# Kernel tuning notes

Measured on AMD Instinct MI355X. Metric: run time of the kernel, lower is better.

The kernel has to match this reference:

```python
import jax, jax.numpy as jnp
import numpy as np
from jax import lax

NPOINT = 1024
NSAMPLES = (16, 32, 64)
BN_EPS = 1e-5


def fps(xyz, npoint):
    """Farthest point sampling. xyz: [B,N,3] -> idx [B,npoint].
    Deterministic start at index 0 (torch version uses a random start)."""
    B, N, _ = xyz.shape

    def step(carry, _):
        dist, far = carry
        centroid = jnp.take_along_axis(xyz, far[:, None, None], axis=1)  # [B,1,3]
        d = jnp.sum((xyz - centroid) ** 2, axis=-1)                      # [B,N]
        dist = jnp.minimum(dist, d)
        nxt = jnp.argmax(dist, axis=1)
        return (dist, nxt), far

    init = (jnp.full((B, N), 1e10, xyz.dtype), jnp.zeros((B,), jnp.int32))
    _, idxs = lax.scan(step, init, None, length=npoint)  # [npoint,B]
    return idxs.T


def gather_points(points, idx):
    # points [B,N,C], idx [B,...] -> [B,...,C]
    return jax.vmap(lambda p, i: p[i])(points, idx)


def sq_cdist(a, b):
    # a [B,S,3], b [B,N,3] -> squared distances [B,S,N] (same ordering as cdist)
    aa = jnp.sum(a * a, -1)[:, :, None]
    bb = jnp.sum(b * b, -1)[:, None, :]
    return aa + bb - 2.0 * jnp.einsum('bsc,bnc->bsn', a, b)


def mlp_scale(g, ws, gs, bs):
    # g: [B,S,k,Cin]; 1x1 conv + BatchNorm (training-mode stats) + ReLU per layer
    for w, gm, bt in zip(ws, gs, bs):
        g = jnp.einsum('bskc,oc->bsko', g, w)
        mu = jnp.mean(g, axis=(0, 1, 2))
        var = jnp.var(g, axis=(0, 1, 2))
        g = jax.nn.relu((g - mu) * lax.rsqrt(var + BN_EPS) * gm + bt)
    return g


def setup_inputs() -> dict:
    key = jax.random.key(0)
    ks = jax.random.split(key, 16)
    B, N, C = 16, 4096, 64
    xyz = jax.random.normal(ks[0], (B, N, 3), jnp.float32)
    features = jax.random.normal(ks[1], (B, N, C), jnp.float32)
    # stacked per-scale MLP params; layer dims: 67 -> 64 -> 64 -> 128
    w0 = jax.random.normal(ks[2], (3, 64, 67), jnp.float32) * 0.1
    w1 = jax.random.normal(ks[3], (3, 64, 64), jnp.float32) * 0.1
    w2 = jax.random.normal(ks[4], (3, 128, 64), jnp.float32) * 0.1
    g0 = jnp.ones((3, 64), jnp.float32); b0 = jnp.zeros((3, 64), jnp.float32)
    g1 = jnp.ones((3, 64), jnp.float32); b1 = jnp.zeros((3, 64), jnp.float32)
    g2 = jnp.ones((3, 128), jnp.float32); b2 = jnp.zeros((3, 128), jnp.float32)
    return {"xyz": xyz, "features": features, "w0": w0, "w1": w1, "w2": w2,
            "g0": g0, "g1": g1, "g2": g2, "b0": b0, "b1": b1, "b2": b2}


def reference(xyz, features, w0, w1, w2, g0, g1, g2, b0, b1, b2):
    fps_idx = fps(xyz, NPOINT)                                   # [B,S]
    new_xyz = jnp.take_along_axis(xyz, fps_idx[..., None], axis=1)  # [B,S,3]
    d2 = sq_cdist(new_xyz, xyz)                                  # [B,S,N]
    outs = []
    for s, nsample in enumerate(NSAMPLES):
        _, idx = lax.top_k(-d2, nsample)                         # k nearest, [B,S,k]
        grouped_xyz = gather_points(xyz, idx) - new_xyz[:, :, None, :]
        grouped_f = gather_points(features, idx)
        g = jnp.concatenate([grouped_xyz, grouped_f], axis=-1)   # [B,S,k,67]
        g = mlp_scale(g, (w0[s], w1[s], w2[s]), (g0[s], g1[s], g2[s]), (b0[s], b1[s], b2[s]))
        outs.append(jnp.max(g, axis=2))                          # max over neighbors -> [B,S,128]
    fused = jnp.concatenate(outs, axis=-1)                       # [B,S,384]
    return new_xyz, fused
```

## Files before the change

kernel.cpp:

```cpp
#include <hip/hip_runtime.h>
#include <stdint.h>

#define BATCH 16
#define NPTS  4096
#define NSAMP 1024

typedef __attribute__((ext_vector_type(8))) short  short8;
typedef __attribute__((ext_vector_type(4))) float  floatx4;

__device__ __forceinline__ unsigned short f2bf(float f) {
    unsigned u = __float_as_uint(f);
    unsigned r = (u + 0x7FFFu + ((u >> 16) & 1u)) >> 16;
    return (unsigned short)r;
}

template<int CTRL>
__device__ __forceinline__ uint64_t dpp_max_u64(uint64_t k) {
    int lo = (int)(unsigned)k;
    int hi = (int)(unsigned)(k >> 32);
    int lo2 = __builtin_amdgcn_update_dpp(0, lo, CTRL, 0xF, 0xF, false);
    int hi2 = __builtin_amdgcn_update_dpp(0, hi, CTRL, 0xF, 0xF, false);
    uint64_t o = ((uint64_t)(unsigned)hi2 << 32) | (unsigned)lo2;
    return o > k ? o : k;
}

__global__ __launch_bounds__(512) void fps_conv_kernel(
    const float* __restrict__ xyz,
    float* __restrict__ out_xyz,
    const float* __restrict__ feat,
    unsigned short* __restrict__ featb,
    int staged)
{
#pragma clang fp contract(off)
    if (blockIdx.x >= 16) {
        if (staged) {
            int t = (blockIdx.x - 16) * 512 + threadIdx.x;
            const float4* fp = (const float4*)feat + (size_t)t*2;
            float4 a = fp[0], c = fp[1];
            uint4 o;
            o.x = (unsigned)f2bf(a.x) | ((unsigned)f2bf(a.y) << 16);
            o.y = (unsigned)f2bf(a.z) | ((unsigned)f2bf(a.w) << 16);
            o.z = (unsigned)f2bf(c.x) | ((unsigned)f2bf(c.y) << 16);
            o.w = (unsigned)f2bf(c.z) | ((unsigned)f2bf(c.w) << 16);
            ((uint4*)featb)[t] = o;
        }
        return;
    }

    const int b    = blockIdx.x;
    const int tid  = threadIdx.x;
    const int lane = tid & 63;
    const int wave = tid >> 6;
    const float* xb = xyz + (size_t)b * NPTS * 3;

    __shared__ float xsh[NPTS], ysh[NPTS], zsh[NPTS];
    __shared__ float cents[NSAMP * 3];
    __shared__ uint64_t keylds[2][8];

    float px[8], py[8], pz[8], dist[8];
    unsigned nidx[8];
#pragma unroll
    for (int i = 0; i < 8; ++i) {
        int p = tid + (i << 9);
        px[i] = xb[p*3+0];
        py[i] = xb[p*3+1];
        pz[i] = xb[p*3+2];
        dist[i] = 1e10f;
        nidx[i] = ~(unsigned)p;
        xsh[p] = px[i]; ysh[p] = py[i]; zsh[p] = pz[i];
    }
    __syncthreads();

    float cx = xb[0], cy = xb[1], cz = xb[2];

    for (int it = 0; it < NSAMP; ++it) {
        if (tid == 0) {
            cents[it*3+0] = cx; cents[it*3+1] = cy; cents[it*3+2] = cz;
        }
        if (it == NSAMP - 1) break;

        uint64_t k[8];
#pragma unroll
        for (int i = 0; i < 8; ++i) {
            float dx = px[i] - cx, dy = py[i] - cy, dz = pz[i] - cz;
            float d = dx*dx; d = d + dy*dy; d = d + dz*dz;
            float nd = fminf(dist[i], d);
            dist[i] = nd;
            k[i] = ((uint64_t)__float_as_uint(nd) << 32) | nidx[i];
        }
        uint64_t m0 = k[0] > k[1] ? k[0] : k[1];
        uint64_t m1 = k[2] > k[3] ? k[2] : k[3];
        uint64_t m2 = k[4] > k[5] ? k[4] : k[5];
        uint64_t m3 = k[6] > k[7] ? k[6] : k[7];
        uint64_t ma = m0 > m1 ? m0 : m1;
        uint64_t mb = m2 > m3 ? m2 : m3;
        uint64_t kk = ma > mb ? ma : mb;

        kk = dpp_max_u64<0x121>(kk);
        kk = dpp_max_u64<0x122>(kk);
        kk = dpp_max_u64<0x124>(kk);
        kk = dpp_max_u64<0x128>(kk);
        kk = dpp_max_u64<0x142>(kk);
        kk = dpp_max_u64<0x143>(kk);

        int pb = it & 1;
        if (lane == 63) keylds[pb][wave] = kk;
        __syncthreads();

        uint64_t f = keylds[pb][lane & 7];
        f = dpp_max_u64<0x121>(f);
        f = dpp_max_u64<0x122>(f);
        f = dpp_max_u64<0x124>(f);
        int cur = (int)~((unsigned)f);

        cx = xsh[cur]; cy = ysh[cur]; cz = zsh[cur];
    }

    __syncthreads();
    for (int i = tid; i < NSAMP*3; i += 512)
        out_xyz[(size_t)b*NSAMP*3 + i] = cents[i];
}

#define WT_S 18432

__global__ __launch_bounds__(256) void conv_w_kernel(
    const float* __restrict__ w0, const float* __restrict__ w1,
    const float* __restrict__ w2, unsigned short* __restrict__ wtab)
{
    int t = blockIdx.x * 256 + threadIdx.x;
    if (t >= 3*WT_S) return;
    int s = t / WT_S, r = t % WT_S;
    unsigned short v = 0;
    if (r < 6144) {
        int n = r / 96, kg = r % 96;
        if (kg < 67) {
            int ci = (kg < 64) ? (kg + 3) : (kg - 64);
            v = f2bf(w0[(size_t)(s*64 + n)*67 + ci]);
        }
    } else if (r < 10240) {
        int idx = r - 6144;
        v = f2bf(w1[(size_t)(s*64 + (idx >> 6))*64 + (idx & 63)]);
    } else {
        int idx = r - 10240;
        v = f2bf(w2[(size_t)(s*128 + (idx >> 6))*64 + (idx & 63)]);
    }
    wtab[t] = v;
}

__global__ __launch_bounds__(256) void knn_kernel(
    const float* __restrict__ xyz,
    const float* __restrict__ new_xyz,
    unsigned short* __restrict__ knn_idx)
{
#pragma clang fp contract(off)
    __shared__ float xs[NPTS], ys[NPTS], zs[NPTS];
    __shared__ uint64_t buf[4][64];
    const int tid  = threadIdx.x;
    const int lane = tid & 63;
    const int wave = tid >> 6;
    const int q = blockIdx.x * 4 + wave;
    const int b = q >> 10;
    const float* xb = xyz + (size_t)b * NPTS * 3;

    for (int i = tid; i < NPTS; i += 256) {
        xs[i] = xb[i*3+0];
        ys[i] = xb[i*3+1];
        zs[i] = xb[i*3+2];
    }
    __syncthreads();

    const float qx = new_xyz[q*3+0], qy = new_xyz[q*3+1], qz = new_xyz[q*3+2];
    float aa = qx*qx; aa = aa + qy*qy; aa = aa + qz*qz;

    auto keyof = [&](int c) -> unsigned {
        float x = xs[c], y = ys[c], z = zs[c];
        float bb = x*x;  bb = bb + y*y;   bb = bb + z*z;
        float dt = qx*x; dt = dt + qy*y;  dt = dt + qz*z;
        float d2 = (aa + bb) - 2.0f*dt;
        unsigned u = __float_as_uint(d2);
        return (u & 0x80000000u) ? ~u : (u | 0x80000000u);
    };
    auto shfl64 = [&](uint64_t v, int src) -> uint64_t {
        int lo = __shfl((int)(unsigned)v, src);
        int hi = __shfl((int)(unsigned)(v >> 32), src);
        return ((uint64_t)(unsigned)hi << 32) | (unsigned)lo;
    };
    auto shflx64 = [&](uint64_t v, int m) -> uint64_t {
        int lo = __shfl_xor((int)(unsigned)v, m);
        int hi = __shfl_xor((int)(unsigned)(v >> 32), m);
        return ((uint64_t)(unsigned)hi << 32) | (unsigned)lo;
    };
    auto sortP = [&](uint64_t &p) {
#pragma unroll
        for (int kk = 2; kk <= 64; kk <<= 1) {
#pragma unroll
            for (int j = kk >> 1; j >= 1; j >>= 1) {
                uint64_t o = shflx64(p, j);
                bool up    = ((lane & kk) == 0);
                bool lower = ((lane & j) == 0);
                bool oless = o < p;
                bool keep  = (up == lower) ? oless : !oless;
                if (keep) p = o;
            }
        }
    };
    auto mergeP = [&](uint64_t &P, uint64_t Bv) {
        uint64_t rev = shfl64(Bv, 63 - lane);
        if (rev < P) P = rev;
#pragma unroll
        for (int j = 32; j >= 1; j >>= 1) {
            uint64_t o = shflx64(P, j);
            bool lower = ((lane & j) == 0);
            bool oless = o < P;
            bool keep  = lower ? oless : !oless;
            if (keep) P = o;
        }
    };

    uint64_t P = ((uint64_t)keyof(lane) << 32) | (unsigned)lane;
    sortP(P);
    uint64_t Pmax = shfl64(P, 63);
    int cnt = 0;

    for (int bt = 1; bt < 64; ++bt) {
        int c = (bt << 6) + lane;
        uint64_t cand = ((uint64_t)keyof(c) << 32) | (unsigned)c;
        bool qual = cand < Pmax;
        unsigned long long mask = __ballot(qual);
        if (mask == 0ull) continue;
        int n = __popcll(mask);
        if (cnt + n > 64) {
            uint64_t Bv = (lane < cnt) ? buf[wave][lane] : ~0ull;
            sortP(Bv);
            mergeP(P, Bv);
            Pmax = shfl64(P, 63);
            cnt = 0;
            qual = qual && (cand < Pmax);
            mask = __ballot(qual);
            n = __popcll(mask);
        }
        if (qual) {
            int pos = cnt + __popcll(mask & ((1ull << lane) - 1ull));
            buf[wave][pos] = cand;
        }
        cnt += n;
    }
    if (cnt > 0) {
        uint64_t Bv = (lane < cnt) ? buf[wave][lane] : ~0ull;
        sortP(Bv);
        mergeP(P, Bv);
    }
    knn_idx[(size_t)q*64 + lane] = (unsigned short)(P & 0xFFFFu);
}

#define GPB 8

template<int PHASE>
__global__ __launch_bounds__(256) void mlp_phase(
    const float* __restrict__ xyz,
    const float* __restrict__ feat,
    const float* __restrict__ new_xyz,
    const unsigned short* __restrict__ knn,
    const unsigned short* __restrict__ featb,
    int staged,
    const unsigned short* __restrict__ wtab,
    const float* __restrict__ bnp,
    float* __restrict__ stats,
    float* __restrict__ out1)
{
    __shared__ __align__(16) unsigned short g_lds[64*104];
    __shared__ __align__(16) unsigned short a_lds[64*72];
    __shared__ float stat_lds[256];
    __shared__ float wavemax[4*128];

    const int tid  = threadIdx.x;
    const int lane = tid & 63;
    const int wave = tid >> 6;
    const int n16  = lane & 15;
    const int quad = lane >> 4;

    int scale, g0;
    {
        int blk = blockIdx.x;
        if (blk < 512)       { scale = 0; g0 = blk * GPB; }
        else if (blk < 1536) { scale = 1; g0 = (blk - 512) * GPB; }
        else                 { scale = 2; g0 = (blk - 1536) * GPB; }
    }
    const int KNB = 16 << scale;
    const int cpg = 4 >> scale;
    const int wpc = 1 << scale;

    const unsigned short* wt  = wtab + scale * WT_S;
    const unsigned short* w2b = wt + 6144;
    const unsigned short* w3b = wt + 10240;

    short8 w1f[4][3];
#pragma unroll
    for (int nt = 0; nt < 4; ++nt)
#pragma unroll
        for (int kb = 0; kb < 3; ++kb)
            w1f[nt][kb] = *(const short8*)&wt[(nt*16 + n16)*96 + kb*32 + quad*8];

    float s1p[4], t1p[4], s2p[4], t2p[4];
    if constexpr (PHASE >= 2) {
#pragma unroll
        for (int nt = 0; nt < 4; ++nt) {
            int o = ((0*3 + scale)*128 + nt*16 + n16)*2;
            s1p[nt] = bnp[o]; t1p[nt] = bnp[o+1];
        }
    }
    if constexpr (PHASE >= 3) {
#pragma unroll
        for (int nt = 0; nt < 4; ++nt) {
            int o = ((1*3 + scale)*128 + nt*16 + n16)*2;
            s2p[nt] = bnp[o]; t2p[nt] = bnp[o+1];
        }
    }

    float sac[8], sqac[8];
#pragma unroll
    for (int i = 0; i < 8; ++i) { sac[i] = 0.f; sqac[i] = 0.f; }
    stat_lds[tid] = 0.f;
    {
        const int r = tid >> 2;
        const int sub = tid & 3;
        if (sub == 0)      *(uint4*)&g_lds[r*104 + 72] = make_uint4(0u,0u,0u,0u);
        else if (sub == 1) *(uint4*)&g_lds[r*104 + 80] = make_uint4(0u,0u,0u,0u);
        else if (sub == 2) *(uint4*)&g_lds[r*104 + 88] = make_uint4(0u,0u,0u,0u);
    }
    __syncthreads();

    for (int g = g0; g < g0 + GPB; ++g) {
        const int cb = g * cpg;
        {
            const int r   = tid >> 2;
            const int sub = tid & 3;
            const int ci  = cb + (r >> (4 + scale));
            const int j   = r & (KNB - 1);
            const int n   = knn[(size_t)ci*64 + j];
            const int b   = ci >> 10;
            if (staged) {
                const unsigned short* frow = featb + ((size_t)(b*NPTS + n))*64 + sub*16;
                uint4 c0 = ((const uint4*)frow)[0];
                uint4 c1 = ((const uint4*)frow)[1];
                *(uint4*)&g_lds[r*104 + sub*16]     = c0;
                *(uint4*)&g_lds[r*104 + sub*16 + 8] = c1;
            } else {
                const float* frow = feat + ((size_t)(b*NPTS + n))*64 + sub*16;
                unsigned short h[16];
#pragma unroll
                for (int u = 0; u < 16; ++u) h[u] = f2bf(frow[u]);
                uint4 p0, p1;
                p0.x = (unsigned)h[0]  | ((unsigned)h[1]  << 16);
                p0.y = (unsigned)h[2]  | ((unsigned)h[3]  << 16);
                p0.z = (unsigned)h[4]  | ((unsigned)h[5]  << 16);
                p0.w = (unsigned)h[6]  | ((unsigned)h[7]  << 16);
                p1.x = (unsigned)h[8]  | ((unsigned)h[9]  << 16);
                p1.y = (unsigned)h[10] | ((unsigned)h[11] << 16);
                p1.z = (unsigned)h[12] | ((unsigned)h[13] << 16);
                p1.w = (unsigned)h[14] | ((unsigned)h[15] << 16);
                *(uint4*)&g_lds[r*104 + sub*16]     = p0;
                *(uint4*)&g_lds[r*104 + sub*16 + 8] = p1;
            }
            if (sub == 0) {
                const float* nx = new_xyz + (size_t)ci*3;
                const float* xp = xyz + ((size_t)(b*NPTS + n))*3;
                unsigned short h0 = f2bf(xp[0] - nx[0]);
                unsigned short h1 = f2bf(xp[1] - nx[1]);
                unsigned short h2 = f2bf(xp[2] - nx[2]);
                uint4 z = make_uint4((unsigned)h0 | ((unsigned)h1 << 16),
                                     (unsigned)h2, 0u, 0u);
                *(uint4*)&g_lds[r*104 + 64] = z;
            }
        }
        __syncthreads();

        const int rb = wave*16 + n16;
        short8 a0 = *(const short8*)&g_lds[rb*104 +      quad*8];
        short8 a1 = *(const short8*)&g_lds[rb*104 + 32 + quad*8];
        short8 a2 = *(const short8*)&g_lds[rb*104 + 64 + quad*8];
        floatx4 acc[4];
#pragma unroll
        for (int nt = 0; nt < 4; ++nt) {
            floatx4 c = {0.f,0.f,0.f,0.f};
            c = __builtin_amdgcn_mfma_f32_16x16x32_bf16(a0, w1f[nt][0], c, 0,0,0);
            c = __builtin_amdgcn_mfma_f32_16x16x32_bf16(a1, w1f[nt][1], c, 0,0,0);
            c = __builtin_amdgcn_mfma_f32_16x16x32_bf16(a2, w1f[nt][2], c, 0,0,0);
            acc[nt] = c;
        }

        if constexpr (PHASE == 1) {
#pragma unroll
            for (int nt = 0; nt < 4; ++nt) {
                floatx4 c = acc[nt];
                sac[nt]  += c[0]+c[1]+c[2]+c[3];
                sqac[nt] += c[0]*c[0]+c[1]*c[1]+c[2]*c[2]+c[3]*c[3];
            }
        }
        if constexpr (PHASE >= 2) {
#pragma unroll
            for (int nt = 0; nt < 4; ++nt) {
                int ch = nt*16 + n16;
#pragma unroll
                for (int r = 0; r < 4; ++r) {
                    float v = acc[nt][r]*s1p[nt] + t1p[nt];
                    v = fmaxf(v, 0.f);
                    a_lds[(wave*16 + quad*4 + r)*72 + ch] = f2bf(v);
                }
            }
            short8 e0 = *(const short8*)&a_lds[rb*72 +      quad*8];
            short8 e1 = *(const short8*)&a_lds[rb*72 + 32 + quad*8];
            floatx4 acc2[4];
#pragma unroll
            for (int nt = 0; nt < 4; ++nt) {
                short8 wa = *(const short8*)&w2b[(nt*16 + n16)*64 +      quad*8];
                short8 wb = *(const short8*)&w2b[(nt*16 + n16)*64 + 32 + quad*8];
                floatx4 c = {0.f,0.f,0.f,0.f};
                c = __builtin_amdgcn_mfma_f32_16x16x32_bf16(e0, wa, c, 0,0,0);
                c = __builtin_amdgcn_mfma_f32_16x16x32_bf16(e1, wb, c, 0,0,0);
                acc2[nt] = c;
            }
            if constexpr (PHASE == 2) {
#pragma unroll
                for (int nt = 0; nt < 4; ++nt) {
                    floatx4 c = acc2[nt];
                    sac[nt]  += c[0]+c[1]+c[2]+c[3];
                    sqac[nt] += c[0]*c[0]+c[1]*c[1]+c[2]*c[2]+c[3]*c[3];
                }
            }
            if constexpr (PHASE == 3) {
#pragma unroll
                for (int nt = 0; nt < 4; ++nt) {
                    int ch = nt*16 + n16;
#pragma unroll
                    for (int r = 0; r < 4; ++r) {
                        float v = acc2[nt][r]*s2p[nt] + t2p[nt];
                        v = fmaxf(v, 0.f);
                        a_lds[(wave*16 + quad*4 + r)*72 + ch] = f2bf(v);
                    }
                }
                short8 f0 = *(const short8*)&a_lds[rb*72 +      quad*8];
                short8 f1 = *(const short8*)&a_lds[rb*72 + 32 + quad*8];
#pragma unroll
                for (int nt = 0; nt < 8; ++nt) {
                    short8 wa = *(const short8*)&w3b[(nt*16 + n16)*64 +      quad*8];
                    short8 wb = *(const short8*)&w3b[(nt*16 + n16)*64 + 32 + quad*8];
                    floatx4 c = {0.f,0.f,0.f,0.f};
                    c = __builtin_amdgcn_mfma_f32_16x16x32_bf16(f0, wa, c, 0,0,0);
                    c = __builtin_amdgcn_mfma_f32_16x16x32_bf16(f1, wb, c, 0,0,0);
                    sac[nt]  += c[0]+c[1]+c[2]+c[3];
                    sqac[nt] += c[0]*c[0]+c[1]*c[1]+c[2]*c[2]+c[3]*c[3];
                    float m = fmaxf(fmaxf(c[0],c[1]), fmaxf(c[2],c[3]));
                    m = fmaxf(m, __shfl_xor(m, 16));
                    m = fmaxf(m, __shfl_xor(m, 32));
                    if (lane < 16) wavemax[wave*128 + nt*16 + n16] = m;
                }
            }
        }
        __syncthreads();
        if constexpr (PHASE == 3) {
            const int ch = tid & 127;
            for (int ic = tid >> 7; ic < cpg; ic += 2) {
                float m = wavemax[(ic*wpc)*128 + ch];
                for (int w = 1; w < wpc; ++w)
                    m = fmaxf(m, wavemax[(ic*wpc + w)*128 + ch]);
                out1[(size_t)(cb + ic)*384 + scale*128 + ch] = m;
            }
        }
    }

    const int NCH = (PHASE == 3) ? 8 : 4;
#pragma unroll
    for (int nt = 0; nt < 8; ++nt) {
        if (nt >= NCH) break;
        float v  = sac[nt], v2 = sqac[nt];
        v  += __shfl_xor(v, 16);  v  += __shfl_xor(v, 32);
        v2 += __shfl_xor(v2, 16); v2 += __shfl_xor(v2, 32);
        if (lane < 16) {
            int ch = nt*16 + n16;
            atomicAdd(&stat_lds[ch*2],   v);
            atomicAdd(&stat_lds[ch*2+1], v2);
        }
    }
    __syncthreads();
    const int layer = PHASE - 1;
    const int nch = (PHASE == 3) ? 128 : 64;
    if (tid < nch*2) {
        atomicAdd(&stats[(size_t)(layer*3 + scale)*256 + tid], stat_lds[tid]);
    }
}

__global__ void bn_params_kernel(
    const float* __restrict__ stats, float* __restrict__ bnp,
    const float* __restrict__ gamma, const float* __restrict__ beta,
    int layer, int nch)
{
    int t = blockIdx.x * blockDim.x + threadIdx.x;
    if (t >= 3*nch) return;
    int scale = t / nch, ch = t % nch;
    float M = 16384.0f * (float)(16 << scale);
    int o = ((layer*3 + scale)*128 + ch)*2;
    float sum = stats[o], sumsq = stats[o+1];
    float mean = sum / M;
    float var = sumsq / M - mean*mean;
    var = fmaxf(var, 0.f);
    float ga = gamma[scale*nch + ch];
    float be = beta[scale*nch + ch];
    float s  = ga / sqrtf(var + 1e-5f);
    float tt = be - mean * s;
    bnp[o] = s; bnp[o+1] = tt;
}

__global__ void finalize_kernel(
    const float* __restrict__ bnp,
    float* __restrict__ out1)
{
    int t = blockIdx.x * 256 + threadIdx.x;
    float4 m = ((const float4*)out1)[t];
    int c0 = (t*4) % 384;
    int scale = c0 >> 7;
    int ch = c0 & 127;
    int o = ((2*3 + scale)*128 + ch)*2;
    float4 r;
    r.x = fmaxf(m.x*bnp[o+0] + bnp[o+1], 0.f);
    r.y = fmaxf(m.y*bnp[o+2] + bnp[o+3], 0.f);
    r.z = fmaxf(m.z*bnp[o+4] + bnp[o+5], 0.f);
    r.w = fmaxf(m.w*bnp[o+6] + bnp[o+7], 0.f);
    ((float4*)out1)[t] = r;
}

extern "C" void kernel_launch(void* const* d_in, const int* in_sizes, int n_in,
                              void* d_out, int out_size, void* d_ws, size_t ws_size,
                              hipStream_t stream)
{
    (void)in_sizes; (void)n_in; (void)out_size;
    const float* xyz  = (const float*)d_in[0];
    const float* feat = (const float*)d_in[1];
    const float* w0   = (const float*)d_in[2];
    const float* w1   = (const float*)d_in[3];
    const float* w2   = (const float*)d_in[4];
    const float* g0   = (const float*)d_in[5];
    const float* g1   = (const float*)d_in[6];
    const float* g2   = (const float*)d_in[7];
    const float* b0   = (const float*)d_in[8];
    const float* b1   = (const float*)d_in[9];
    const float* b2   = (const float*)d_in[10];
    float* out  = (float*)d_out;
    float* out0 = out;
    float* out1 = out + 49152;

    char* ws = (char*)d_ws;
    const size_t NEED_FULL = 2097152ull + 8388608ull + 9216 + 9216 + 110592;
    const int staged = (ws_size >= NEED_FULL) ? 1 : 0;
    unsigned short* knn   = (unsigned short*)ws;
    unsigned short* featb = staged ? (unsigned short*)(ws + 2097152) : nullptr;
    size_t tail = staged ? (2097152ull + 8388608ull) : 2097152ull;
    float* stats = (float*)(ws + tail);
    float* bnp   = (float*)(ws + tail + 9216);
    unsigned short* wtab = (unsigned short*)(ws + tail + 18432);

    hipMemsetAsync(stats, 0, 9216, stream);
    fps_conv_kernel<<<16 + (staged ? 1024 : 0), 512, 0, stream>>>(
        xyz, out0, feat, featb, staged);
    conv_w_kernel<<<216, 256, 0, stream>>>(w0, w1, w2, wtab);
    knn_kernel<<<4096, 256, 0, stream>>>(xyz, out0, knn);

    mlp_phase<1><<<3584,256,0,stream>>>(xyz,feat,out0,knn,featb,staged,wtab,bnp,stats,out1);
    bn_params_kernel<<<1,256,0,stream>>>(stats, bnp, g0, b0, 0, 64);

    mlp_phase<2><<<3584,256,0,stream>>>(xyz,feat,out0,knn,featb,staged,wtab,bnp,stats,out1);
    bn_params_kernel<<<1,256,0,stream>>>(stats, bnp, g1, b1, 1, 64);

    mlp_phase<3><<<3584,256,0,stream>>>(xyz,feat,out0,knn,featb,staged,wtab,bnp,stats,out1);
    bn_params_kernel<<<2,256,0,stream>>>(stats, bnp, g2, b2, 2, 128);

    finalize_kernel<<<6144, 256, 0, stream>>>(bnp, out1);
}
```

Before: 1.422 ms.

## Process all three scales per query in one block, sharing gathered neighbor rows

Blocks are reorganized so each block handles whole queries, and all three scales are computed from a single 64-neighbor gather in LDS. The 16 and 32 nearest neighbors are prefixes of the 64, so waves 0-3 run scale 2 while waves 0-2 also run scales 1 and 0 on the leading rows. This removes the redundant neighbor-feature gathers that were repeated for each scale. In exchange, weights are no longer held in registers but read from global memory inside the task, wave 3 has less work than the others, and LDS use per block grows.

```diff
diff --git a/kernel.cpp b/kernel.cpp
--- a/kernel.cpp
+++ b/kernel.cpp
@@ -253,7 +253,7 @@
     knn_idx[(size_t)q*64 + lane] = (unsigned short)(P & 0xFFFFu);
 }
 
-#define GPB 8
+#define GPB 4
 
 template<int PHASE>
 __global__ __launch_bounds__(256) void mlp_phase(
@@ -269,9 +269,9 @@
     float* __restrict__ out1)
 {
     __shared__ __align__(16) unsigned short g_lds[64*104];
-    __shared__ __align__(16) unsigned short a_lds[64*72];
-    __shared__ float stat_lds[256];
-    __shared__ float wavemax[4*128];
+    __shared__ __align__(16) unsigned short a_lds[112*72];
+    __shared__ float stat_lds[3*256];
+    __shared__ float wavemax[7*128];
 
     const int tid  = threadIdx.x;
     const int lane = tid & 63;
@@ -279,48 +279,21 @@
     const int n16  = lane & 15;
     const int quad = lane >> 4;
 
-    int scale, g0;
-    {
-        int blk = blockIdx.x;
-        if (blk < 512)       { scale = 0; g0 = blk * GPB; }
-        else if (blk < 1536) { scale = 1; g0 = (blk - 512) * GPB; }
-        else                 { scale = 2; g0 = (blk - 1536) * GPB; }
-    }
-    const int KNB = 16 << scale;
-    const int cpg = 4 >> scale;
-    const int wpc = 1 << scale;
-
-    const unsigned short* wt  = wtab + scale * WT_S;
-    const unsigned short* w2b = wt + 6144;
-    const unsigned short* w3b = wt + 10240;
-
-    short8 w1f[4][3];
-#pragma unroll
-    for (int nt = 0; nt < 4; ++nt)
-#pragma unroll
-        for (int kb = 0; kb < 3; ++kb)
-            w1f[nt][kb] = *(const short8*)&wt[(nt*16 + n16)*96 + kb*32 + quad*8];
-
-    float s1p[4], t1p[4], s2p[4], t2p[4];
-    if constexpr (PHASE >= 2) {
-#pragma unroll
-        for (int nt = 0; nt < 4; ++nt) {
-            int o = ((0*3 + scale)*128 + nt*16 + n16)*2;
-            s1p[nt] = bnp[o]; t1p[nt] = bnp[o+1];
-        }
-    }
-    if constexpr (PHASE >= 3) {
-#pragma unroll
-        for (int nt = 0; nt < 4; ++nt) {
-            int o = ((1*3 + scale)*128 + nt*16 + n16)*2;
-            s2p[nt] = bnp[o]; t2p[nt] = bnp[o+1];
-        }
-    }
-
-    float sac[8], sqac[8];
-#pragma unroll
-    for (int i = 0; i < 8; ++i) { sac[i] = 0.f; sqac[i] = 0.f; }
-    stat_lds[tid] = 0.f;
+    const int  sA  = 2;
+    const int  rbA = wave*16;
+    const int  arA = wave*16;
+    const int  wsA = wave;
+    const bool hasB = (wave < 3);
+    const int  sB  = (wave < 2) ? 1 : 0;
+    const int  rbB = (wave == 1) ? 16 : 0;
+    const int  arB = 64 + wave*16;
+    const int  wsB = 4 + wave;
+
+    float sacA[8], sqacA[8], sacB[8], sqacB[8];
+#pragma unroll
+    for (int i = 0; i < 8; ++i) { sacA[i]=0.f; sqacA[i]=0.f; sacB[i]=0.f; sqacB[i]=0.f; }
+
+    for (int i = tid; i < 3*256; i += 256) stat_lds[i] = 0.f;
     {
         const int r = tid >> 2;
         const int sub = tid & 3;
@@ -328,17 +301,106 @@
         else if (sub == 1) *(uint4*)&g_lds[r*104 + 80] = make_uint4(0u,0u,0u,0u);
         else if (sub == 2) *(uint4*)&g_lds[r*104 + 88] = make_uint4(0u,0u,0u,0u);
     }
-    __syncthreads();
-
-    for (int g = g0; g < g0 + GPB; ++g) {
-        const int cb = g * cpg;
+
+    auto run_task = [&](int sc, int rb_rows, int arow, int wslot,
+                        float* sac, float* sqac) {
+        const unsigned short* wt  = wtab + sc * WT_S;
+        const unsigned short* w2b = wt + 6144;
+        const unsigned short* w3b = wt + 10240;
+        const int gr = (rb_rows + n16)*104;
+        short8 a0 = *(const short8*)&g_lds[gr +      quad*8];
+        short8 a1 = *(const short8*)&g_lds[gr + 32 + quad*8];
+        short8 a2 = *(const short8*)&g_lds[gr + 64 + quad*8];
+        floatx4 acc[4];
+#pragma unroll
+        for (int nt = 0; nt < 4; ++nt) {
+            const unsigned short* wr = &wt[(nt*16 + n16)*96 + quad*8];
+            floatx4 c = {0.f,0.f,0.f,0.f};
+            c = __builtin_amdgcn_mfma_f32_16x16x32_bf16(a0, *(const short8*)&wr[0],  c, 0,0,0);
+            c = __builtin_amdgcn_mfma_f32_16x16x32_bf16(a1, *(const short8*)&wr[32], c, 0,0,0);
+            c = __builtin_amdgcn_mfma_f32_16x16x32_bf16(a2, *(const short8*)&wr[64], c, 0,0,0);
+            acc[nt] = c;
+        }
+        if constexpr (PHASE == 1) {
+#pragma unroll
+            for (int nt = 0; nt < 4; ++nt) {
+                floatx4 c = acc[nt];
+                sac[nt]  += c[0]+c[1]+c[2]+c[3];
+                sqac[nt] += c[0]*c[0]+c[1]*c[1]+c[2]*c[2]+c[3]*c[3];
+            }
+            return;
+        } else {
+#pragma unroll
+            for (int nt = 0; nt < 4; ++nt) {
+                int o = ((0*3 + sc)*128 + nt*16 + n16)*2;
+                float s1 = bnp[o], t1 = bnp[o+1];
+                int ch = nt*16 + n16;
+#pragma unroll
+                for (int r = 0; r < 4; ++r) {
+                    float v = acc[nt][r]*s1 + t1;
+                    v = fmaxf(v, 0.f);
+                    a_lds[(arow + quad*4 + r)*72 + ch] = f2bf(v);
+                }
+            }
+            const int ar = (arow + n16)*72;
+            short8 e0 = *(const short8*)&a_lds[ar +      quad*8];
+            short8 e1 = *(const short8*)&a_lds[ar + 32 + quad*8];
+            floatx4 acc2[4];
+#pragma unroll
+            for (int nt = 0; nt < 4; ++nt) {
+                const unsigned short* wr = &w2b[(nt*16 + n16)*64 + quad*8];
+                floatx4 c = {0.f,0.f,0.f,0.f};
+                c = __builtin_amdgcn_mfma_f32_16x16x32_bf16(e0, *(const short8*)&wr[0],  c, 0,0,0);
+                c = __builtin_amdgcn_mfma_f32_16x16x32_bf16(e1, *(const short8*)&wr[32], c, 0,0,0);
+                acc2[nt] = c;
+            }
+            if constexpr (PHASE == 2) {
+#pragma unroll
+                for (int nt = 0; nt < 4; ++nt) {
+                    floatx4 c = acc2[nt];
+                    sac[nt]  += c[0]+c[1]+c[2]+c[3];
+                    sqac[nt] += c[0]*c[0]+c[1]*c[1]+c[2]*c[2]+c[3]*c[3];
+                }
+                return;
+            } else {
+#pragma unroll
+                for (int nt = 0; nt < 4; ++nt) {
+                    int o = ((1*3 + sc)*128 + nt*16 + n16)*2;
+                    float s2 = bnp[o], t2 = bnp[o+1];
+                    int ch = nt*16 + n16;
+#pragma unroll
+                    for (int r = 0; r < 4; ++r) {
+                        float v = acc2[nt][r]*s2 + t2;
+                        v = fmaxf(v, 0.f);
+                        a_lds[(arow + quad*4 + r)*72 + ch] = f2bf(v);
+                    }
+                }
+                short8 f0 = *(const short8*)&a_lds[ar +      quad*8];
+                short8 f1 = *(const short8*)&a_lds[ar + 32 + quad*8];
+#pragma unroll
+                for (int nt = 0; nt < 8; ++nt) {
+                    const unsigned short* wr = &w3b[(nt*16 + n16)*64 + quad*8];
+                    floatx4 c = {0.f,0.f,0.f,0.f};
+                    c = __builtin_amdgcn_mfma_f32_16x16x32_bf16(f0, *(const short8*)&wr[0],  c, 0,0,0);
+                    c = __builtin_amdgcn_mfma_f32_16x16x32_bf16(f1, *(const short8*)&wr[32], c, 0,0,0);
+                    sac[nt]  += c[0]+c[1]+c[2]+c[3];
+                    sqac[nt] += c[0]*c[0]+c[1]*c[1]+c[2]*c[2]+c[3]*c[3];
+                    float m = fmaxf(fmaxf(c[0],c[1]), fmaxf(c[2],c[3]));
+                    m = fmaxf(m, __shfl_xor(m, 16));
+                    m = fmaxf(m, __shfl_xor(m, 32));
+                    if (lane < 16) wavemax[wslot*128 + nt*16 + n16] = m;
+                }
+            }
+        }
+    };
+
+    const int q0 = blockIdx.x * GPB;
+    for (int q = q0; q < q0 + GPB; ++q) {
         {
             const int r   = tid >> 2;
             const int sub = tid & 3;
-            const int ci  = cb + (r >> (4 + scale));
-            const int j   = r & (KNB - 1);
-            const int n   = knn[(size_t)ci*64 + j];
-            const int b   = ci >> 10;
+            const int n   = knn[(size_t)q*64 + r];
+            const int b   = q >> 10;
             if (staged) {
                 const unsigned short* frow = featb + ((size_t)(b*NPTS + n))*64 + sub*16;
                 uint4 c0 = ((const uint4*)frow)[0];
@@ -363,7 +425,7 @@
                 *(uint4*)&g_lds[r*104 + sub*16 + 8] = p1;
             }
             if (sub == 0) {
-                const float* nx = new_xyz + (size_t)ci*3;
+                const float* nx = new_xyz + (size_t)q*3;
                 const float* xp = xyz + ((size_t)(b*NPTS + n))*3;
                 unsigned short h0 = f2bf(xp[0] - nx[0]);
                 unsigned short h1 = f2bf(xp[1] - nx[1]);
@@ -375,119 +437,47 @@
         }
         __syncthreads();
 
-        const int rb = wave*16 + n16;
-        short8 a0 = *(const short8*)&g_lds[rb*104 +      quad*8];
-        short8 a1 = *(const short8*)&g_lds[rb*104 + 32 + quad*8];
-        short8 a2 = *(const short8*)&g_lds[rb*104 + 64 + quad*8];
-        floatx4 acc[4];
-#pragma unroll
-        for (int nt = 0; nt < 4; ++nt) {
-            floatx4 c = {0.f,0.f,0.f,0.f};
-            c = __builtin_amdgcn_mfma_f32_16x16x32_bf16(a0, w1f[nt][0], c, 0,0,0);
-            c = __builtin_amdgcn_mfma_f32_16x16x32_bf16(a1, w1f[nt][1], c, 0,0,0);
-            c = __builtin_amdgcn_mfma_f32_16x16x32_bf16(a2, w1f[nt][2], c, 0,0,0);
-            acc[nt] = c;
-        }
-
-        if constexpr (PHASE == 1) {
-#pragma unroll
-            for (int nt = 0; nt < 4; ++nt) {
-                floatx4 c = acc[nt];
-                sac[nt]  += c[0]+c[1]+c[2]+c[3];
-                sqac[nt] += c[0]*c[0]+c[1]*c[1]+c[2]*c[2]+c[3]*c[3];
-            }
-        }
-        if constexpr (PHASE >= 2) {
-#pragma unroll
-            for (int nt = 0; nt < 4; ++nt) {
-                int ch = nt*16 + n16;
-#pragma unroll
-                for (int r = 0; r < 4; ++r) {
-                    float v = acc[nt][r]*s1p[nt] + t1p[nt];
-                    v = fmaxf(v, 0.f);
-                    a_lds[(wave*16 + quad*4 + r)*72 + ch] = f2bf(v);
-                }
-            }
-            short8 e0 = *(const short8*)&a_lds[rb*72 +      quad*8];
-            short8 e1 = *(const short8*)&a_lds[rb*72 + 32 + quad*8];
-            floatx4 acc2[4];
-#pragma unroll
-            for (int nt = 0; nt < 4; ++nt) {
-                short8 wa = *(const short8*)&w2b[(nt*16 + n16)*64 +      quad*8];
-                short8 wb = *(const short8*)&w2b[(nt*16 + n16)*64 + 32 + quad*8];
-                floatx4 c = {0.f,0.f,0.f,0.f};
-                c = __builtin_amdgcn_mfma_f32_16x16x32_bf16(e0, wa, c, 0,0,0);
-                c = __builtin_amdgcn_mfma_f32_16x16x32_bf16(e1, wb, c, 0,0,0);
-                acc2[nt] = c;
-            }
-            if constexpr (PHASE == 2) {
-#pragma unroll
-                for (int nt = 0; nt < 4; ++nt) {
-                    floatx4 c = acc2[nt];
-                    sac[nt]  += c[0]+c[1]+c[2]+c[3];
-                    sqac[nt] += c[0]*c[0]+c[1]*c[1]+c[2]*c[2]+c[3]*c[3];
-                }
-            }
-            if constexpr (PHASE == 3) {
-#pragma unroll
-                for (int nt = 0; nt < 4; ++nt) {
-                    int ch = nt*16 + n16;
-#pragma unroll
-                    for (int r = 0; r < 4; ++r) {
-                        float v = acc2[nt][r]*s2p[nt] + t2p[nt];
-                        v = fmaxf(v, 0.f);
-                        a_lds[(wave*16 + quad*4 + r)*72 + ch] = f2bf(v);
-                    }
-                }
-                short8 f0 = *(const short8*)&a_lds[rb*72 +      quad*8];
-                short8 f1 = *(const short8*)&a_lds[rb*72 + 32 + quad*8];
-#pragma unroll
-                for (int nt = 0; nt < 8; ++nt) {
-                    short8 wa = *(const short8*)&w3b[(nt*16 + n16)*64 +      quad*8];
-                    short8 wb = *(const short8*)&w3b[(nt*16 + n16)*64 + 32 + quad*8];
-                    floatx4 c = {0.f,0.f,0.f,0.f};
-                    c = __builtin_amdgcn_mfma_f32_16x16x32_bf16(f0, wa, c, 0,0,0);
-                    c = __builtin_amdgcn_mfma_f32_16x16x32_bf16(f1, wb, c, 0,0,0);
-                    sac[nt]  += c[0]+c[1]+c[2]+c[3];
-                    sqac[nt] += c[0]*c[0]+c[1]*c[1]+c[2]*c[2]+c[3]*c[3];
-                    float m = fmaxf(fmaxf(c[0],c[1]), fmaxf(c[2],c[3]));
-                    m = fmaxf(m, __shfl_xor(m, 16));
-                    m = fmaxf(m, __shfl_xor(m, 32));
-                    if (lane < 16) wavemax[wave*128 + nt*16 + n16] = m;
-                }
-            }
-        }
+        run_task(sA, rbA, arA, wsA, sacA, sqacA);
+        if (hasB) run_task(sB, rbB, arB, wsB, sacB, sqacB);
+
         __syncthreads();
         if constexpr (PHASE == 3) {
-            const int ch = tid & 127;
-            for (int ic = tid >> 7; ic < cpg; ic += 2) {
-                float m = wavemax[(ic*wpc)*128 + ch];
-                for (int w = 1; w < wpc; ++w)
-                    m = fmaxf(m, wavemax[(ic*wpc + w)*128 + ch]);
-                out1[(size_t)(cb + ic)*384 + scale*128 + ch] = m;
+            for (int t = tid; t < 384; t += 256) {
+                int sc = t >> 7, ch = t & 127;
+                float m;
+                if (sc == 2)
+                    m = fmaxf(fmaxf(wavemax[0*128+ch], wavemax[1*128+ch]),
+                              fmaxf(wavemax[2*128+ch], wavemax[3*128+ch]));
+                else if (sc == 1)
+                    m = fmaxf(wavemax[4*128+ch], wavemax[5*128+ch]);
+                else
+                    m = wavemax[6*128+ch];
+                out1[(size_t)q*384 + t] = m;
             }
         }
     }
 
     const int NCH = (PHASE == 3) ? 8 : 4;
-#pragma unroll
-    for (int nt = 0; nt < 8; ++nt) {
-        if (nt >= NCH) break;
-        float v  = sac[nt], v2 = sqac[nt];
-        v  += __shfl_xor(v, 16);  v  += __shfl_xor(v, 32);
-        v2 += __shfl_xor(v2, 16); v2 += __shfl_xor(v2, 32);
-        if (lane < 16) {
-            int ch = nt*16 + n16;
-            atomicAdd(&stat_lds[ch*2],   v);
-            atomicAdd(&stat_lds[ch*2+1], v2);
-        }
-    }
+    auto flush = [&](int sc, float* sac, float* sqac) {
+#pragma unroll
+        for (int nt = 0; nt < 8; ++nt) {
+            if (nt >= NCH) break;
+            float v  = sac[nt], v2 = sqac[nt];
+            v  += __shfl_xor(v, 16);  v  += __shfl_xor(v, 32);
+            v2 += __shfl_xor(v2, 16); v2 += __shfl_xor(v2, 32);
+            if (lane < 16) {
+                int ch = nt*16 + n16;
+                atomicAdd(&stat_lds[sc*256 + ch*2],   v);
+                atomicAdd(&stat_lds[sc*256 + ch*2+1], v2);
+            }
+        }
+    };
+    flush(sA, sacA, sqacA);
+    if (hasB) flush(sB, sacB, sqacB);
     __syncthreads();
     const int layer = PHASE - 1;
-    const int nch = (PHASE == 3) ? 128 : 64;
-    if (tid < nch*2) {
-        atomicAdd(&stats[(size_t)(layer*3 + scale)*256 + tid], stat_lds[tid]);
-    }
+    for (int t = tid; t < 3*256; t += 256)
+        atomicAdd(&stats[(size_t)layer*768 + t], stat_lds[t]);
 }
 
 __global__ void bn_params_kernel(
@@ -565,13 +555,13 @@
     conv_w_kernel<<<216, 256, 0, stream>>>(w0, w1, w2, wtab);
     knn_kernel<<<4096, 256, 0, stream>>>(xyz, out0, knn);
 
-    mlp_phase<1><<<3584,256,0,stream>>>(xyz,feat,out0,knn,featb,staged,wtab,bnp,stats,out1);
+    mlp_phase<1><<<4096,256,0,stream>>>(xyz,feat,out0,knn,featb,staged,wtab,bnp,stats,out1);
     bn_params_kernel<<<1,256,0,stream>>>(stats, bnp, g0, b0, 0, 64);
 
-    mlp_phase<2><<<3584,256,0,stream>>>(xyz,feat,out0,knn,featb,staged,wtab,bnp,stats,out1);
+    mlp_phase<2><<<4096,256,0,stream>>>(xyz,feat,out0,knn,featb,staged,wtab,bnp,stats,out1);
     bn_params_kernel<<<1,256,0,stream>>>(stats, bnp, g1, b1, 1, 64);
 
-    mlp_phase<3><<<3584,256,0,stream>>>(xyz,feat,out0,knn,featb,staged,wtab,bnp,stats,out1);
+    mlp_phase<3><<<4096,256,0,stream>>>(xyz,feat,out0,knn,featb,staged,wtab,bnp,stats,out1);
     bn_params_kernel<<<2,256,0,stream>>>(stats, bnp, g2, b2, 2, 128);
 
     finalize_kernel<<<6144, 256, 0, stream>>>(bnp, out1);
```

Result: slower. 1.987 ms (+39.7%).
